# Optimization experiments

Hardware: AMD Instinct MI355X
Metric: run time of the kernel (lower is better)

## Reference

```python
import jax, jax.numpy as jnp
import numpy as np

N = 100000      # atoms
P = 6400000     # pairs (~64 neighbors/atom)
T = 16          # atom types
BOX_L = 30.0    # cubic box edge (Angstrom)


def setup_inputs() -> dict:
    key = jax.random.key(0)
    k_c, k_i, k_off, k_a, k_b, k_t = jax.random.split(key, 6)
    coords = jax.random.uniform(k_c, (N, 3), dtype=jnp.float32) * BOX_L
    # build pairs with i != j so distances are never exactly zero
    i = jax.random.randint(k_i, (P,), 0, N)
    off = jax.random.randint(k_off, (P,), 1, N)
    j = (i + off) % N
    pairs = jnp.stack([i, j], axis=1).astype(jnp.int64)
    box = (BOX_L * jnp.eye(3)).astype(jnp.float32)
    A = jax.random.uniform(k_a, (T, T), dtype=jnp.float32)
    B = jax.random.uniform(k_b, (T, T), dtype=jnp.float32) + 0.5
    atom_types = jax.random.randint(k_t, (N,), 0, T).astype(jnp.int64)
    return {
        "coords": coords,
        "pairs": pairs,
        "box": box,
        "A": A,
        "B": B,
        "cutoff": 12,
        "atom_types": atom_types,
    }


def reference(coords, pairs, box, A, B, cutoff, atom_types):
    # gather pair endpoints: (P,3)
    dr = coords[pairs[:, 1]] - coords[pairs[:, 0]]
    # minimum-image convention (general triclinic box): fractional wrap
    inv_box = jnp.linalg.inv(box)
    s = dr @ inv_box
    s = s - jnp.round(s)
    dr_vecs = s @ box
    r = jnp.linalg.norm(dr_vecs, axis=1)          # (P,)
    # type-pair indexed amplitudes / inverse lengths
    ti = atom_types[pairs[:, 0]]
    tj = atom_types[pairs[:, 1]]
    A_ij = A[ti, tj]
    B_ij = B[ti, tj]
    # Slater energy: x = B r, Pfac = x^2/3 + x + 1, E = A * Pfac * exp(-x)
    x = B_ij * r
    Pfac = x * x / 3.0 + x + 1.0
    ene = A_ij * Pfac * jnp.exp(-x)
    ene = jnp.where(r <= jnp.float32(cutoff), ene, 0.0)
    return jnp.sum(ene)
```

## Files before the change

### kernel.cpp

```cpp
#include <hip/hip_runtime.h>


#ifndef SLATER_T
#define SLATER_T 16
#endif

__global__ __launch_bounds__(256)
void repack_kernel(const float* __restrict__ coords,
                   const int* __restrict__ types,
                   const float* __restrict__ A,
                   const float* __restrict__ B,
                   float4* __restrict__ packed,
                   float2* __restrict__ abt,
                   float* __restrict__ out, int out_size,
                   int n)
{
    int i = blockIdx.x * blockDim.x + threadIdx.x;
    if (i < out_size) out[i] = 0.0f;
    if (i < SLATER_T * SLATER_T) abt[i] = make_float2(A[i], B[i]);
    int stride = gridDim.x * blockDim.x;
    for (; i < n; i += stride) {
        float4 v;
        v.x = coords[3 * i + 0];
        v.y = coords[3 * i + 1];
        v.z = coords[3 * i + 2];
        v.w = __int_as_float(types[i]);
        packed[i] = v;
    }
}

__global__ __launch_bounds__(256)
void zero_kernel(float* __restrict__ out, int out_size)
{
    int i = blockIdx.x * blockDim.x + threadIdx.x;
    if (i < out_size) out[i] = 0.0f;
}

template <bool PACKED>
__global__ __launch_bounds__(256)
void slater_kernel(const int* __restrict__ pairs,
                   const float4* __restrict__ packed,
                   const float2* __restrict__ abt,
                   const float* __restrict__ coords,
                   const int* __restrict__ types,
                   const float* __restrict__ A,
                   const float* __restrict__ B,
                   const float* __restrict__ box,
                   const int* __restrict__ cutoffp,
                   float* __restrict__ out,
                   int nP)
{
    float b00 = box[0], b01 = box[1], b02 = box[2];
    float b10 = box[3], b11 = box[4], b12 = box[5];
    float b20 = box[6], b21 = box[7], b22 = box[8];

    float C00 =  (b11 * b22 - b12 * b21);
    float C01 = -(b10 * b22 - b12 * b20);
    float C02 =  (b10 * b21 - b11 * b20);
    float C10 = -(b01 * b22 - b02 * b21);
    float C11 =  (b00 * b22 - b02 * b20);
    float C12 = -(b00 * b21 - b01 * b20);
    float C20 =  (b01 * b12 - b02 * b11);
    float C21 = -(b00 * b12 - b02 * b10);
    float C22 =  (b00 * b11 - b01 * b10);
    float det = b00 * C00 + b01 * C01 + b02 * C02;
    float inv_det = 1.0f / det;
    float i00 = C00 * inv_det, i01 = C10 * inv_det, i02 = C20 * inv_det;
    float i10 = C01 * inv_det, i11 = C11 * inv_det, i12 = C21 * inv_det;
    float i20 = C02 * inv_det, i21 = C12 * inv_det, i22 = C22 * inv_det;

    float cut = (float)(*cutoffp);

    float acc = 0.0f;
    int tid    = blockIdx.x * blockDim.x + threadIdx.x;
    int stride = gridDim.x * blockDim.x;

    auto body = [&](int ia, int ja) {
        float ax, ay, az, bx, by, bz;
        int ti, tj;
        if (PACKED) {
            float4 ca = packed[ia];
            float4 cb = packed[ja];
            ax = ca.x; ay = ca.y; az = ca.z; ti = __float_as_int(ca.w);
            bx = cb.x; by = cb.y; bz = cb.z; tj = __float_as_int(cb.w);
        } else {
            ax = coords[3 * ia + 0]; ay = coords[3 * ia + 1]; az = coords[3 * ia + 2];
            bx = coords[3 * ja + 0]; by = coords[3 * ja + 1]; bz = coords[3 * ja + 2];
            ti = types[ia];
            tj = types[ja];
        }

        float dx = bx - ax, dy = by - ay, dz = bz - az;

        float s0 = dx * i00 + dy * i10 + dz * i20;
        float s1 = dx * i01 + dy * i11 + dz * i21;
        float s2 = dx * i02 + dy * i12 + dz * i22;
        s0 -= rintf(s0);
        s1 -= rintf(s1);
        s2 -= rintf(s2);
        float d0 = s0 * b00 + s1 * b10 + s2 * b20;
        float d1 = s0 * b01 + s1 * b11 + s2 * b21;
        float d2 = s0 * b02 + s1 * b12 + s2 * b22;

        float r = sqrtf(d0 * d0 + d1 * d1 + d2 * d2);

        float Aij, Bij;
        if (PACKED) {
            float2 abv = abt[ti * SLATER_T + tj];
            Aij = abv.x; Bij = abv.y;
        } else {
            Aij = A[ti * SLATER_T + tj];
            Bij = B[ti * SLATER_T + tj];
        }

        float x  = Bij * r;
        float pf = x * x * (1.0f / 3.0f) + x + 1.0f;
        float e  = Aij * pf * __expf(-x);
        acc += (r <= cut) ? e : 0.0f;
    };

    const int4* p4 = (const int4*)pairs;
    int n4 = nP >> 1;
    for (int p = tid; p < n4; p += stride) {
        int4 pr = p4[p];
        body(pr.x, pr.y);
        body(pr.z, pr.w);
    }
    if (tid == 0 && (nP & 1)) {
        body(pairs[2 * (nP - 1)], pairs[2 * (nP - 1) + 1]);
    }

    #pragma unroll
    for (int off = 32; off > 0; off >>= 1)
        acc += __shfl_down(acc, off, 64);

    __shared__ float wsum[4];
    int lane = threadIdx.x & 63;
    int wid  = threadIdx.x >> 6;
    if (lane == 0) wsum[wid] = acc;
    __syncthreads();
    if (threadIdx.x == 0) {
        float s = wsum[0] + wsum[1] + wsum[2] + wsum[3];
        atomicAdd(out, s);
    }
}

extern "C" void kernel_launch(void* const* d_in, const int* in_sizes, int n_in,
                              void* d_out, int out_size, void* d_ws, size_t ws_size,
                              hipStream_t stream)
{
    const float* coords = (const float*)d_in[0];
    const int*   pairs  = (const int*)d_in[1];
    const float* box    = (const float*)d_in[2];
    const float* A      = (const float*)d_in[3];
    const float* B      = (const float*)d_in[4];
    const int*   cutoff = (const int*)d_in[5];
    const int*   types  = (const int*)d_in[6];

    int n  = in_sizes[0] / 3;
    int nP = in_sizes[1] / 2;

    float* out = (float*)d_out;

    size_t packed_bytes = (size_t)n * sizeof(float4);
    size_t need = packed_bytes + (size_t)(SLATER_T * SLATER_T) * sizeof(float2);

    const int THREADS = 256;
    const int BLOCKS  = 2048;

    if (ws_size >= need) {
        float4* packed = (float4*)d_ws;
        float2* abt    = (float2*)((char*)d_ws + packed_bytes);
        int rblocks = (n + THREADS - 1) / THREADS;
        if (rblocks > 2048) rblocks = 2048;
        repack_kernel<<<rblocks, THREADS, 0, stream>>>(coords, types, A, B, packed, abt,
                                                       out, out_size, n);
        slater_kernel<true><<<BLOCKS, THREADS, 0, stream>>>(
            pairs, packed, abt,
            nullptr, nullptr, nullptr, nullptr,
            box, cutoff, out, nP);
    } else {
        zero_kernel<<<(out_size + THREADS - 1) / THREADS, THREADS, 0, stream>>>(out, out_size);
        slater_kernel<false><<<BLOCKS, THREADS, 0, stream>>>(
            pairs, nullptr, nullptr,
            coords, types, A, B,
            box, cutoff, out, nP);
    }
}
```

Measured before the change: 71.88 us.

## Bucket-sort pairs into atom tiles and compute from shared-memory coordinate tiles

Adds a per-call counting sort of the pair list into 2D buckets of 2048-atom tiles (histogram, single-block scan, scatter). A compute kernel then runs one block per bucket and reads coordinates and types from two shared-memory tiles instead of doing random global gathers. The aim is to remove the latency of scattered per-pair coordinate loads. In exchange the pair array is read several more times and written once to workspace, and a serial single-block scan sits on the critical path. The fallback path gets a 2x unrolled gather loop with the A/B table in shared memory.

```diff
diff --git a/kernel.cpp b/kernel.cpp
--- a/kernel.cpp
+++ b/kernel.cpp
@@ -1,149 +1,297 @@
 #include <hip/hip_runtime.h>
 
 
-#ifndef SLATER_T
-#define SLATER_T 16
-#endif
-
-__global__ __launch_bounds__(256)
-void repack_kernel(const float* __restrict__ coords,
-                   const int* __restrict__ types,
-                   const float* __restrict__ A,
-                   const float* __restrict__ B,
-                   float4* __restrict__ packed,
-                   float2* __restrict__ abt,
-                   float* __restrict__ out, int out_size,
-                   int n)
-{
-    int i = blockIdx.x * blockDim.x + threadIdx.x;
-    if (i < out_size) out[i] = 0.0f;
-    if (i < SLATER_T * SLATER_T) abt[i] = make_float2(A[i], B[i]);
-    int stride = gridDim.x * blockDim.x;
-    for (; i < n; i += stride) {
-        float4 v;
-        v.x = coords[3 * i + 0];
-        v.y = coords[3 * i + 1];
-        v.z = coords[3 * i + 2];
-        v.w = __int_as_float(types[i]);
-        packed[i] = v;
-    }
-}
-
-__global__ __launch_bounds__(256)
-void zero_kernel(float* __restrict__ out, int out_size)
-{
-    int i = blockIdx.x * blockDim.x + threadIdx.x;
-    if (i < out_size) out[i] = 0.0f;
-}
-
-template <bool PACKED>
-__global__ __launch_bounds__(256)
-void slater_kernel(const int* __restrict__ pairs,
-                   const float4* __restrict__ packed,
-                   const float2* __restrict__ abt,
-                   const float* __restrict__ coords,
-                   const int* __restrict__ types,
-                   const float* __restrict__ A,
-                   const float* __restrict__ B,
-                   const float* __restrict__ box,
-                   const int* __restrict__ cutoffp,
-                   float* __restrict__ out,
-                   int nP)
-{
-    float b00 = box[0], b01 = box[1], b02 = box[2];
-    float b10 = box[3], b11 = box[4], b12 = box[5];
-    float b20 = box[6], b21 = box[7], b22 = box[8];
-
-    float C00 =  (b11 * b22 - b12 * b21);
-    float C01 = -(b10 * b22 - b12 * b20);
-    float C02 =  (b10 * b21 - b11 * b20);
-    float C10 = -(b01 * b22 - b02 * b21);
-    float C11 =  (b00 * b22 - b02 * b20);
-    float C12 = -(b00 * b21 - b01 * b20);
-    float C20 =  (b01 * b12 - b02 * b11);
-    float C21 = -(b00 * b12 - b02 * b10);
-    float C22 =  (b00 * b11 - b01 * b10);
-    float det = b00 * C00 + b01 * C01 + b02 * C02;
-    float inv_det = 1.0f / det;
-    float i00 = C00 * inv_det, i01 = C10 * inv_det, i02 = C20 * inv_det;
-    float i10 = C01 * inv_det, i11 = C11 * inv_det, i12 = C21 * inv_det;
-    float i20 = C02 * inv_det, i21 = C12 * inv_det, i22 = C22 * inv_det;
-
+#define TT     16
+#define S_LOG  11
+#define S_TILE 2048
+#define MAXNB  2560
+#define NPB    512
+
+typedef unsigned int u32;
+
+struct BoxMats {
+    float b00,b01,b02,b10,b11,b12,b20,b21,b22;
+    float i00,i01,i02,i10,i11,i12,i20,i21,i22;
+};
+
+__device__ inline BoxMats load_box(const float* __restrict__ box) {
+    BoxMats m;
+    m.b00=box[0]; m.b01=box[1]; m.b02=box[2];
+    m.b10=box[3]; m.b11=box[4]; m.b12=box[5];
+    m.b20=box[6]; m.b21=box[7]; m.b22=box[8];
+    float C00 =  (m.b11*m.b22 - m.b12*m.b21);
+    float C01 = -(m.b10*m.b22 - m.b12*m.b20);
+    float C02 =  (m.b10*m.b21 - m.b11*m.b20);
+    float C10 = -(m.b01*m.b22 - m.b02*m.b21);
+    float C11 =  (m.b00*m.b22 - m.b02*m.b20);
+    float C12 = -(m.b00*m.b21 - m.b01*m.b20);
+    float C20 =  (m.b01*m.b12 - m.b02*m.b11);
+    float C21 = -(m.b00*m.b12 - m.b02*m.b10);
+    float C22 =  (m.b00*m.b11 - m.b01*m.b10);
+    float det = m.b00*C00 + m.b01*C01 + m.b02*C02;
+    float inv = 1.0f/det;
+    m.i00=C00*inv; m.i01=C10*inv; m.i02=C20*inv;
+    m.i10=C01*inv; m.i11=C11*inv; m.i12=C21*inv;
+    m.i20=C02*inv; m.i21=C12*inv; m.i22=C22*inv;
+    return m;
+}
+
+__device__ inline float pair_energy(const BoxMats& m, float4 ca, float4 cb,
+                                    float Aij, float Bij, float cut) {
+    float dx = cb.x-ca.x, dy = cb.y-ca.y, dz = cb.z-ca.z;
+    float s0 = dx*m.i00 + dy*m.i10 + dz*m.i20;
+    float s1 = dx*m.i01 + dy*m.i11 + dz*m.i21;
+    float s2 = dx*m.i02 + dy*m.i12 + dz*m.i22;
+    s0 -= rintf(s0); s1 -= rintf(s1); s2 -= rintf(s2);
+    float d0 = s0*m.b00 + s1*m.b10 + s2*m.b20;
+    float d1 = s0*m.b01 + s1*m.b11 + s2*m.b21;
+    float d2 = s0*m.b02 + s1*m.b12 + s2*m.b22;
+    float r  = sqrtf(d0*d0 + d1*d1 + d2*d2);
+    float x  = Bij*r;
+    float pf = x*x*(1.0f/3.0f) + x + 1.0f;
+    float e  = Aij*pf*__expf(-x);
+    return (r <= cut) ? e : 0.0f;
+}
+
+__global__ __launch_bounds__(256)
+void zero_kernel(u32* __restrict__ bucketTot, int nb)
+{
+    int i = blockIdx.x*blockDim.x + threadIdx.x;
+    if (i < nb) bucketTot[i] = 0u;
+}
+
+__global__ __launch_bounds__(256)
+void hist_kernel(const int2* __restrict__ pairs, u32* __restrict__ bucketTot,
+                 int nP, int G, int perBlk)
+{
+    __shared__ u32 h[MAXNB];
+    int nb = G*G;
+    for (int t = threadIdx.x; t < nb; t += 256) h[t] = 0u;
+    __syncthreads();
+    int lo = blockIdx.x*perBlk;
+    int hi = min(nP, lo + perBlk);
+    for (int p = lo + threadIdx.x; p < hi; p += 256) {
+        int2 pr = pairs[p];
+        int b = (pr.x >> S_LOG)*G + (pr.y >> S_LOG);
+        atomicAdd(&h[b], 1u);
+    }
+    __syncthreads();
+    for (int t = threadIdx.x; t < nb; t += 256)
+        if (h[t]) atomicAdd(&bucketTot[t], h[t]);
+}
+
+__global__ __launch_bounds__(1024)
+void scan_kernel(const u32* __restrict__ bucketTot,
+                 u32* __restrict__ bucketStart, u32* __restrict__ bucketCursor,
+                 float2* __restrict__ abt, const float* __restrict__ A,
+                 const float* __restrict__ B,
+                 float* __restrict__ out, int outN, int nb)
+{
+    __shared__ u32 part[1024];
+    int t = threadIdx.x;
+    int chunk = (nb + 1023) >> 10;
+    int lo = t*chunk, hi = min(nb, lo + chunk);
+    u32 s = 0;
+    for (int k = lo; k < hi; k++) s += bucketTot[k];
+    part[t] = s;
+    __syncthreads();
+    for (int off = 1; off < 1024; off <<= 1) {
+        u32 x = part[t];
+        u32 y = (t >= off) ? part[t-off] : 0u;
+        __syncthreads();
+        part[t] = x + y;
+        __syncthreads();
+    }
+    u32 base = (t == 0) ? 0u : part[t-1];
+    for (int k = lo; k < hi; k++) {
+        u32 v = bucketTot[k];
+        bucketStart[k]  = base;
+        bucketCursor[k] = base;
+        base += v;
+    }
+    if (t == 1023) bucketStart[nb] = part[1023];
+    if (t < TT*TT) abt[t] = make_float2(A[t], B[t]);
+    for (int k = t; k < outN; k += 1024) out[k] = 0.0f;
+}
+
+__global__ __launch_bounds__(256)
+void scatter_kernel(const int2* __restrict__ pairs, int2* __restrict__ pairs2,
+                    u32* __restrict__ bucketCursor, int nP, int G, int perBlk)
+{
+    __shared__ u32 h[MAXNB];
+    int nb = G*G;
+    for (int t = threadIdx.x; t < nb; t += 256) h[t] = 0u;
+    __syncthreads();
+    int lo = blockIdx.x*perBlk;
+    int hi = min(nP, lo + perBlk);
+    for (int p = lo + threadIdx.x; p < hi; p += 256) {
+        int2 pr = pairs[p];
+        int b = (pr.x >> S_LOG)*G + (pr.y >> S_LOG);
+        atomicAdd(&h[b], 1u);
+    }
+    __syncthreads();
+    for (int t = threadIdx.x; t < nb; t += 256) {
+        u32 c = h[t];
+        h[t] = c ? atomicAdd(&bucketCursor[t], c) : 0u;
+    }
+    __syncthreads();
+    for (int p = lo + threadIdx.x; p < hi; p += 256) {
+        int2 pr = pairs[p];
+        int b = (pr.x >> S_LOG)*G + (pr.y >> S_LOG);
+        u32 slot = atomicAdd(&h[b], 1u);
+        pairs2[slot] = pr;
+    }
+}
+
+__global__ __launch_bounds__(256)
+void compute_kernel(const int2* __restrict__ pairs2,
+                    const float* __restrict__ coords,
+                    const int* __restrict__ types,
+                    const float2* __restrict__ abt,
+                    const float* __restrict__ box,
+                    const int* __restrict__ cutoffp,
+                    const u32* __restrict__ bucketStart,
+                    float* __restrict__ out, int n, int G)
+{
+    __shared__ float4 tI[S_TILE];
+    __shared__ float4 tJ[S_TILE];
+
+    int b  = blockIdx.x;
+    int bi = b / G;
+    int bj = b - bi*G;
+    int baseI = bi << S_LOG;
+    int baseJ = bj << S_LOG;
+
+    for (int t = threadIdx.x; t < S_TILE; t += 256) {
+        int a = baseI + t;
+        float4 v = make_float4(0.f,0.f,0.f,0.f);
+        if (a < n) v = make_float4(coords[3*a], coords[3*a+1], coords[3*a+2],
+                                   __int_as_float(types[a]));
+        tI[t] = v;
+        int a2 = baseJ + t;
+        float4 w = make_float4(0.f,0.f,0.f,0.f);
+        if (a2 < n) w = make_float4(coords[3*a2], coords[3*a2+1], coords[3*a2+2],
+                                    __int_as_float(types[a2]));
+        tJ[t] = w;
+    }
+    __syncthreads();
+
+    BoxMats m = load_box(box);
     float cut = (float)(*cutoffp);
 
+    u32 lo = bucketStart[b], hi = bucketStart[b+1];
     float acc = 0.0f;
-    int tid    = blockIdx.x * blockDim.x + threadIdx.x;
-    int stride = gridDim.x * blockDim.x;
-
-    auto body = [&](int ia, int ja) {
-        float ax, ay, az, bx, by, bz;
-        int ti, tj;
-        if (PACKED) {
-            float4 ca = packed[ia];
-            float4 cb = packed[ja];
-            ax = ca.x; ay = ca.y; az = ca.z; ti = __float_as_int(ca.w);
-            bx = cb.x; by = cb.y; bz = cb.z; tj = __float_as_int(cb.w);
-        } else {
-            ax = coords[3 * ia + 0]; ay = coords[3 * ia + 1]; az = coords[3 * ia + 2];
-            bx = coords[3 * ja + 0]; by = coords[3 * ja + 1]; bz = coords[3 * ja + 2];
-            ti = types[ia];
-            tj = types[ja];
-        }
-
-        float dx = bx - ax, dy = by - ay, dz = bz - az;
-
-        float s0 = dx * i00 + dy * i10 + dz * i20;
-        float s1 = dx * i01 + dy * i11 + dz * i21;
-        float s2 = dx * i02 + dy * i12 + dz * i22;
-        s0 -= rintf(s0);
-        s1 -= rintf(s1);
-        s2 -= rintf(s2);
-        float d0 = s0 * b00 + s1 * b10 + s2 * b20;
-        float d1 = s0 * b01 + s1 * b11 + s2 * b21;
-        float d2 = s0 * b02 + s1 * b12 + s2 * b22;
-
-        float r = sqrtf(d0 * d0 + d1 * d1 + d2 * d2);
-
-        float Aij, Bij;
-        if (PACKED) {
-            float2 abv = abt[ti * SLATER_T + tj];
-            Aij = abv.x; Bij = abv.y;
-        } else {
-            Aij = A[ti * SLATER_T + tj];
-            Bij = B[ti * SLATER_T + tj];
-        }
-
-        float x  = Bij * r;
-        float pf = x * x * (1.0f / 3.0f) + x + 1.0f;
-        float e  = Aij * pf * __expf(-x);
-        acc += (r <= cut) ? e : 0.0f;
-    };
-
-    const int4* p4 = (const int4*)pairs;
-    int n4 = nP >> 1;
-    for (int p = tid; p < n4; p += stride) {
-        int4 pr = p4[p];
-        body(pr.x, pr.y);
-        body(pr.z, pr.w);
-    }
-    if (tid == 0 && (nP & 1)) {
-        body(pairs[2 * (nP - 1)], pairs[2 * (nP - 1) + 1]);
+    for (u32 p = lo + threadIdx.x; p < hi; p += 256) {
+        int2 pr = pairs2[p];
+        float4 ca = tI[pr.x & (S_TILE-1)];
+        float4 cb = tJ[pr.y & (S_TILE-1)];
+        int ti = __float_as_int(ca.w);
+        int tj = __float_as_int(cb.w);
+        float2 ab = abt[ti*TT + tj];
+        acc += pair_energy(m, ca, cb, ab.x, ab.y, cut);
     }
 
     #pragma unroll
     for (int off = 32; off > 0; off >>= 1)
         acc += __shfl_down(acc, off, 64);
-
+    __syncthreads();
+    float* wsum = (float*)tI;
+    if ((threadIdx.x & 63) == 0) wsum[threadIdx.x >> 6] = acc;
+    __syncthreads();
+    if (threadIdx.x == 0)
+        atomicAdd(out, wsum[0] + wsum[1] + wsum[2] + wsum[3]);
+}
+
+__global__ __launch_bounds__(256)
+void repack_kernel(const float* __restrict__ coords, const int* __restrict__ types,
+                   float4* __restrict__ packed, float* __restrict__ out,
+                   int out_size, int n)
+{
+    int i = blockIdx.x*blockDim.x + threadIdx.x;
+    if (i < out_size) out[i] = 0.0f;
+    int stride = gridDim.x*blockDim.x;
+    for (; i < n; i += stride)
+        packed[i] = make_float4(coords[3*i], coords[3*i+1], coords[3*i+2],
+                                __int_as_float(types[i]));
+}
+
+__global__ __launch_bounds__(256)
+void zero_out_kernel(float* __restrict__ out, int out_size)
+{
+    int i = blockIdx.x*blockDim.x + threadIdx.x;
+    if (i < out_size) out[i] = 0.0f;
+}
+
+__global__ __launch_bounds__(256)
+void slater_unroll(const int* __restrict__ pairs, const float4* __restrict__ packed,
+                   const float* __restrict__ A, const float* __restrict__ B,
+                   const float* __restrict__ box, const int* __restrict__ cutoffp,
+                   float* __restrict__ out, int nP)
+{
+    __shared__ float2 tab[TT*TT];
+    if (threadIdx.x < TT*TT)
+        tab[threadIdx.x] = make_float2(A[threadIdx.x], B[threadIdx.x]);
+    __syncthreads();
+    BoxMats m = load_box(box);
+    float cut = (float)(*cutoffp);
+    float acc = 0.0f;
+    int tid = blockIdx.x*blockDim.x + threadIdx.x;
+    int stride = gridDim.x*blockDim.x;
+    const int4* p4 = (const int4*)pairs;
+    int n4 = nP >> 1;
+    int step = stride*2;
+    int i0 = tid;
+    for (; i0 + stride < n4; i0 += step) {
+        int4 pa = p4[i0];
+        int4 pb = p4[i0 + stride];
+        float4 c0=packed[pa.x], c1=packed[pa.y], c2=packed[pa.z], c3=packed[pa.w];
+        float4 c4=packed[pb.x], c5=packed[pb.y], c6=packed[pb.z], c7=packed[pb.w];
+        {
+            int ti=__float_as_int(c0.w), tj=__float_as_int(c1.w);
+            float2 ab=tab[ti*TT+tj]; acc += pair_energy(m,c0,c1,ab.x,ab.y,cut);
+        }
+        {
+            int ti=__float_as_int(c2.w), tj=__float_as_int(c3.w);
+            float2 ab=tab[ti*TT+tj]; acc += pair_energy(m,c2,c3,ab.x,ab.y,cut);
+        }
+        {
+            int ti=__float_as_int(c4.w), tj=__float_as_int(c5.w);
+            float2 ab=tab[ti*TT+tj]; acc += pair_energy(m,c4,c5,ab.x,ab.y,cut);
+        }
+        {
+            int ti=__float_as_int(c6.w), tj=__float_as_int(c7.w);
+            float2 ab=tab[ti*TT+tj]; acc += pair_energy(m,c6,c7,ab.x,ab.y,cut);
+        }
+    }
+    if (i0 < n4) {
+        int4 pa = p4[i0];
+        float4 c0=packed[pa.x], c1=packed[pa.y], c2=packed[pa.z], c3=packed[pa.w];
+        {
+            int ti=__float_as_int(c0.w), tj=__float_as_int(c1.w);
+            float2 ab=tab[ti*TT+tj]; acc += pair_energy(m,c0,c1,ab.x,ab.y,cut);
+        }
+        {
+            int ti=__float_as_int(c2.w), tj=__float_as_int(c3.w);
+            float2 ab=tab[ti*TT+tj]; acc += pair_energy(m,c2,c3,ab.x,ab.y,cut);
+        }
+    }
+    if (tid == 0 && (nP & 1)) {
+        int ia = pairs[2*(nP-1)], ja = pairs[2*(nP-1)+1];
+        float4 ca = packed[ia], cb = packed[ja];
+        int ti=__float_as_int(ca.w), tj=__float_as_int(cb.w);
+        float2 ab=tab[ti*TT+tj]; acc += pair_energy(m,ca,cb,ab.x,ab.y,cut);
+    }
+    #pragma unroll
+    for (int off = 32; off > 0; off >>= 1)
+        acc += __shfl_down(acc, off, 64);
     __shared__ float wsum[4];
-    int lane = threadIdx.x & 63;
-    int wid  = threadIdx.x >> 6;
-    if (lane == 0) wsum[wid] = acc;
-    __syncthreads();
-    if (threadIdx.x == 0) {
-        float s = wsum[0] + wsum[1] + wsum[2] + wsum[3];
-        atomicAdd(out, s);
-    }
-}
+    if ((threadIdx.x & 63) == 0) wsum[threadIdx.x >> 6] = acc;
+    __syncthreads();
+    if (threadIdx.x == 0)
+        atomicAdd(out, wsum[0]+wsum[1]+wsum[2]+wsum[3]);
+}
+
+static inline size_t align256(size_t x) { return (x + 255) & ~(size_t)255; }
 
 extern "C" void kernel_launch(void* const* d_in, const int* in_sizes, int n_in,
                               void* d_out, int out_size, void* d_ws, size_t ws_size,
@@ -159,31 +307,84 @@
 
     int n  = in_sizes[0] / 3;
     int nP = in_sizes[1] / 2;
-
     float* out = (float*)d_out;
 
-    size_t packed_bytes = (size_t)n * sizeof(float4);
-    size_t need = packed_bytes + (size_t)(SLATER_T * SLATER_T) * sizeof(float2);
-
-    const int THREADS = 256;
-    const int BLOCKS  = 2048;
-
-    if (ws_size >= need) {
+    int G  = (n + S_TILE - 1) >> S_LOG;
+    long nbL = (long)G * G;
+
+    size_t off_p2    = 0;
+    size_t sz_p2     = (size_t)nP * sizeof(int2);
+    size_t off_tot   = align256(off_p2 + sz_p2);
+    size_t off_start = align256(off_tot   + (size_t)MAXNB*4);
+    size_t off_cur   = align256(off_start + (size_t)(MAXNB+1)*4);
+    size_t off_abt   = align256(off_cur   + (size_t)MAXNB*4);
+    size_t need1     = off_abt + TT*TT*sizeof(float2);
+
+    if (nbL <= MAXNB && ws_size >= need1) {
+        int nb = (int)nbL;
+        int2*   pairs2       = (int2*)((char*)d_ws + off_p2);
+        u32*    bucketTot    = (u32*)((char*)d_ws + off_tot);
+        u32*    bucketStart  = (u32*)((char*)d_ws + off_start);
+        u32*    bucketCursor = (u32*)((char*)d_ws + off_cur);
+        float2* abt          = (float2*)((char*)d_ws + off_abt);
+
+        int perBlk = (nP + NPB - 1) / NPB;
+
+        zero_kernel<<<(nb + 255)/256, 256, 0, stream>>>(bucketTot, nb);
+        hist_kernel<<<NPB, 256, 0, stream>>>((const int2*)pairs, bucketTot,
+                                             nP, G, perBlk);
+        scan_kernel<<<1, 1024, 0, stream>>>(bucketTot, bucketStart, bucketCursor,
+                                            abt, A, B, out, out_size, nb);
+        scatter_kernel<<<NPB, 256, 0, stream>>>((const int2*)pairs, pairs2,
+                                                bucketCursor, nP, G, perBlk);
+        compute_kernel<<<nb, 256, 0, stream>>>(pairs2, coords, types, abt, box,
+                                               cutoff, bucketStart, out, n, G);
+    } else if (ws_size >= (size_t)n * sizeof(float4)) {
         float4* packed = (float4*)d_ws;
-        float2* abt    = (float2*)((char*)d_ws + packed_bytes);
-        int rblocks = (n + THREADS - 1) / THREADS;
-        if (rblocks > 2048) rblocks = 2048;
-        repack_kernel<<<rblocks, THREADS, 0, stream>>>(coords, types, A, B, packed, abt,
-                                                       out, out_size, n);
-        slater_kernel<true><<<BLOCKS, THREADS, 0, stream>>>(
-            pairs, packed, abt,
-            nullptr, nullptr, nullptr, nullptr,
-            box, cutoff, out, nP);
+        int rblocks = min(2048, (n + 255)/256);
+        repack_kernel<<<rblocks, 256, 0, stream>>>(coords, types, packed,
+                                                   out, out_size, n);
+        slater_unroll<<<2048, 256, 0, stream>>>(pairs, packed, A, B, box,
+                                                cutoff, out, nP);
     } else {
-        zero_kernel<<<(out_size + THREADS - 1) / THREADS, THREADS, 0, stream>>>(out, out_size);
-        slater_kernel<false><<<BLOCKS, THREADS, 0, stream>>>(
-            pairs, nullptr, nullptr,
-            coords, types, A, B,
-            box, cutoff, out, nP);
-    }
-}
+        zero_out_kernel<<<(out_size + 255)/256, 256, 0, stream>>>(out, out_size);
+        struct Launch { };
+        extern __global__ void slater_simple(const int*, const float*, const int*,
+                                             const float*, const float*, const float*,
+                                             const int*, float*, int);
+        slater_simple<<<2048, 256, 0, stream>>>(pairs, coords, types, A, B, box,
+                                                cutoff, out, nP);
+    }
+}
+
+__global__ __launch_bounds__(256)
+void slater_simple(const int* __restrict__ pairs, const float* __restrict__ coords,
+                   const int* __restrict__ types, const float* __restrict__ A,
+                   const float* __restrict__ B, const float* __restrict__ box,
+                   const int* __restrict__ cutoffp, float* __restrict__ out, int nP)
+{
+    __shared__ float2 tab[TT*TT];
+    if (threadIdx.x < TT*TT)
+        tab[threadIdx.x] = make_float2(A[threadIdx.x], B[threadIdx.x]);
+    __syncthreads();
+    BoxMats m = load_box(box);
+    float cut = (float)(*cutoffp);
+    float acc = 0.0f;
+    int tid = blockIdx.x*blockDim.x + threadIdx.x;
+    int stride = gridDim.x*blockDim.x;
+    for (int p = tid; p < nP; p += stride) {
+        int ia = pairs[2*p], ja = pairs[2*p+1];
+        float4 ca = make_float4(coords[3*ia], coords[3*ia+1], coords[3*ia+2], 0.f);
+        float4 cb = make_float4(coords[3*ja], coords[3*ja+1], coords[3*ja+2], 0.f);
+        float2 ab = tab[types[ia]*TT + types[ja]];
+        acc += pair_energy(m, ca, cb, ab.x, ab.y, cut);
+    }
+    #pragma unroll
+    for (int off = 32; off > 0; off >>= 1)
+        acc += __shfl_down(acc, off, 64);
+    __shared__ float wsum[4];
+    if ((threadIdx.x & 63) == 0) wsum[threadIdx.x >> 6] = acc;
+    __syncthreads();
+    if (threadIdx.x == 0)
+        atomicAdd(out, wsum[0]+wsum[1]+wsum[2]+wsum[3]);
+}
```

Result: slower. 201.2 us (+179.9%).
